# Performance work log

Hardware: AMD Instinct MI355X
Metric: run time of the kernel (lower is better)

## Reference

```python
import jax, jax.numpy as jnp
import numpy as np

HIDDEN = 2048
INTER = 4096
HEADS = 32
HEAD_DIM = INTER // HEADS  # 128
STATE = 128
GROUPS = 1
CONV_K = 4
CHUNK = 256
EPS = 1e-5
CONV_DIM = INTER + 2 * GROUPS * STATE  # 4352
DT_MIN, DT_MAX = 0.0, 100.0
BATCH, SEQ = 2, 4096


def _segment_sum(x):
    """Stable segment sum: returns (..., T, T) with entry [i,j] = sum_{k=j+1..i} x[k] (-inf above diag)."""
    T = x.shape[-1]
    xx = jnp.broadcast_to(x[..., None], x.shape + (T,))
    mask_lower = jnp.tril(jnp.ones((T, T), bool), -1)
    xx = jnp.where(mask_lower, xx, 0.0)
    seg = jnp.cumsum(xx, axis=-2)
    mask_incl = jnp.tril(jnp.ones((T, T), bool), 0)
    return jnp.where(mask_incl, seg, -jnp.inf)


def setup_inputs() -> dict:
    key = jax.random.key(0)
    ks = jax.random.split(key, 8)
    std = 0.02
    return {
        "hidden_states": jax.random.normal(ks[0], (BATCH, SEQ, HIDDEN), jnp.float32),
        "in_proj_w": jax.random.normal(ks[1], (INTER + CONV_DIM + HEADS, HIDDEN), jnp.float32) * std,
        "conv_w": jax.random.normal(ks[2], (CONV_DIM, 1, CONV_K), jnp.float32) * std,
        "conv_b": jnp.zeros((CONV_DIM,), jnp.float32),
        "A_log": jnp.log(jax.random.uniform(ks[3], (HEADS,), jnp.float32, 1.0, 16.0)),
        "dt_bias": jax.random.normal(ks[4], (HEADS,), jnp.float32) * 0.1,
        "D": jnp.ones((HEADS,), jnp.float32),
        "norm_w": jnp.ones((INTER,), jnp.float32),
        "out_proj_w": jax.random.normal(ks[5], (HIDDEN, INTER), jnp.float32) * (std / np.sqrt(48.0)),
    }


def reference(hidden_states, in_proj_w, conv_w, conv_b, A_log, dt_bias, D, norm_w, out_proj_w):
    b, s, _ = hidden_states.shape
    # in_proj and split into gate / conv-input / dt
    proj = hidden_states @ in_proj_w.T
    gate, hBC, dt = jnp.split(proj, [INTER, INTER + CONV_DIM], axis=-1)

    # causal depthwise conv1d (padding k-1 left, truncate to seq_len) + SiLU
    x = jnp.transpose(hBC, (0, 2, 1))  # (b, conv_dim, s)
    x = jax.lax.conv_general_dilated(
        x, conv_w, window_strides=(1,), padding=[(CONV_K - 1, 0)],
        dimension_numbers=("NCH", "OIH", "NCH"), feature_group_count=CONV_DIM)
    x = x + conv_b[None, :, None]
    hBC = jax.nn.silu(jnp.transpose(x, (0, 2, 1)))  # (b, s, conv_dim)

    xs, B, C = jnp.split(hBC, [INTER, INTER + GROUPS * STATE], axis=-1)

    A = -jnp.exp(A_log)  # (h,)
    dt = jnp.clip(jax.nn.softplus(dt + dt_bias), DT_MIN, DT_MAX)  # (b, s, h)

    xs = xs.reshape(b, s, HEADS, HEAD_DIM)
    rep = HEADS // GROUPS
    Bm = jnp.repeat(B.reshape(b, s, GROUPS, STATE), rep, axis=2)  # (b,s,h,n)
    Cm = jnp.repeat(C.reshape(b, s, GROUPS, STATE), rep, axis=2)

    pad = (-s) % CHUNK

    def padseq(t):
        return jnp.pad(t, ((0, 0), (0, pad)) + ((0, 0),) * (t.ndim - 2))

    D_res = D[None, None, :, None] * padseq(xs)  # (b, S, h, p)
    xdt = padseq(xs * dt[..., None])
    Ad = padseq(A[None, None, :] * dt)  # (b, S, h)
    Bm, Cm = padseq(Bm), padseq(Cm)

    nc = (s + pad) // CHUNK
    xdt = xdt.reshape(b, nc, CHUNK, HEADS, HEAD_DIM)
    Ad = jnp.transpose(Ad.reshape(b, nc, CHUNK, HEADS), (0, 3, 1, 2))  # (b,h,c,l)
    Bm = Bm.reshape(b, nc, CHUNK, HEADS, STATE)
    Cm = Cm.reshape(b, nc, CHUNK, HEADS, STATE)

    A_cum = jnp.cumsum(Ad, axis=-1)  # (b,h,c,l)

    # 1) intra-chunk (diagonal block) output
    L = jnp.exp(_segment_sum(Ad))  # (b,h,c,l,l)
    G = jnp.einsum("bclhn,bcshn->bclsh", Cm, Bm)
    M = G * jnp.transpose(L, (0, 2, 3, 4, 1))
    Y_diag = jnp.einsum("bclsh,bcshp->bclhp", M, xdt)

    # 2) per-chunk final states
    decay_states = jnp.exp(A_cum[:, :, :, -1:] - A_cum)  # (b,h,c,l)
    B_decay = Bm * jnp.transpose(decay_states, (0, 2, 3, 1))[..., None]
    states = jnp.einsum("bclhn,bclhp->bchpn", B_decay, xdt)  # (b,c,h,p,n)

    # 3) inter-chunk recurrence
    states = jnp.concatenate([jnp.zeros_like(states[:, :1]), states], axis=1)  # (b,c+1,h,p,n)
    chunk_sums = jnp.pad(A_cum[:, :, :, -1], ((0, 0), (0, 0), (1, 0)))  # (b,h,c+1)
    decay_chunk = jnp.exp(_segment_sum(chunk_sums))  # (b,h,c+1,c+1)
    decay_chunk = jnp.transpose(decay_chunk, (0, 2, 3, 1))  # (b,c,z,h)
    new_states = jnp.einsum("bczh,bchpn->bzhpn", decay_chunk, states)
    states = new_states[:, :-1]  # (b,c,h,p,n) state entering each chunk

    # 4) state -> output contribution
    state_decay = jnp.exp(A_cum)  # (b,h,c,l)
    Y_off = jnp.einsum("bclhn,bchpn->bclhp", Cm, states) * jnp.transpose(state_decay, (0, 2, 3, 1))[..., None]

    y = (Y_diag + Y_off).reshape(b, nc * CHUNK, HEADS, HEAD_DIM) + D_res
    y = y[:, :s].reshape(b, s, INTER)

    # gated RMSNorm
    y = y * jax.nn.silu(gate)
    var = jnp.mean(y * y, axis=-1, keepdims=True)
    y = y * jax.lax.rsqrt(var + EPS) * norm_w

    return y @ out_proj_w.T
```

## Files before the change

kernel.cpp:

```cpp
#include <hip/hip_runtime.h>

#define SEQ     4096
#define BATCH   2
#define NROWS   8192
#define HID     2048
#define INTER_  4096
#define NHEADS  32
#define HDIM    128
#define NSTATE  128
#define CDIM    4352
#define NPROJ_  8480
#define NPAD    8704
#define NCH     16
#define CHUNK_  256

typedef __attribute__((ext_vector_type(8))) short bf16x8;
typedef __attribute__((ext_vector_type(4))) short short4v;
typedef __attribute__((ext_vector_type(4))) float f32x4;

#define AS1 __attribute__((address_space(1)))
#define AS3 __attribute__((address_space(3)))

__device__ __forceinline__ float bf2f(short s) {
  union { unsigned u; float f; } x;
  x.u = ((unsigned)(unsigned short)s) << 16;
  return x.f;
}
__device__ __forceinline__ short f2bf(float f) {
  union { float f; unsigned u; } x; x.f = f;
  unsigned r = x.u + 0x7FFFu + ((x.u >> 16) & 1u);
  return (short)(r >> 16);
}

__global__ void cvt_bf16(const float* __restrict__ in, short* __restrict__ out,
                         int n4, int nsrc4) {
  int i = blockIdx.x * 256 + threadIdx.x;
  if (i >= n4) return;
  short4v o = {0, 0, 0, 0};
  if (i < nsrc4) {
    f32x4 v = *(const f32x4*)(in + (size_t)i * 4);
    o = (short4v){ f2bf(v.x), f2bf(v.y), f2bf(v.z), f2bf(v.w) };
  }
  *(short4v*)(out + (size_t)i * 4) = o;
}

template<int MODE>
__global__ __launch_bounds__(512, 4)
void gemm256(const short* __restrict__ A, const short* __restrict__ Bw,
             int M, int N, int K, int nM,
             float* __restrict__ outF, short* __restrict__ gate,
             short* __restrict__ hbc, float* __restrict__ dtraw)
{
  __shared__ __align__(16) short ldsA[3][256 * 32];
  __shared__ __align__(16) short ldsB[3][128 * 32];
  const int tid = threadIdx.x;
  const int lane = tid & 63, wave = tid >> 6;
  const int l16 = lane & 15, lhi = lane >> 4;
  const int wm = wave >> 1, wn = wave & 1;

  const int bm = blockIdx.x % nM, bn = blockIdx.x / nM;
  const size_t row0 = (size_t)bm * 256;
  const int    col0 = bn * 128;

  const short* Ab  = A + row0 * K;
  const short* Bbp = Bw + (size_t)col0 * K;

  f32x4 acc[4][4];
  #pragma unroll
  for (int m = 0; m < 4; ++m)
    #pragma unroll
    for (int n = 0; n < 4; ++n) acc[m][n] = (f32x4){0.f, 0.f, 0.f, 0.f};

  auto stage = [&](int s) {
    int sl = s % 3;
    short* sa = &ldsA[sl][0];
    short* sb = &ldsB[sl][0];
    int ko = s * 32;
    #pragma unroll
    for (int j = 0; j < 2; ++j) {
      int u = j * 512 + tid;
      int r = u >> 2;
      int q = (u & 3) ^ ((r >> 1) & 3);
      __builtin_amdgcn_global_load_lds(
          (const AS1 unsigned*)(Ab + (size_t)r * K + ko + q * 8),
          (AS3 unsigned*)(sa + (j * 512 + wave * 64) * 8), 16, 0, 0);
    }
    {
      int r = tid >> 2;
      int q = (tid & 3) ^ ((r >> 1) & 3);
      __builtin_amdgcn_global_load_lds(
          (const AS1 unsigned*)(Bbp + (size_t)r * K + ko + q * 8),
          (AS3 unsigned*)(sb + wave * 64 * 8), 16, 0, 0);
    }
  };

  auto compute = [&](int s) {
    int sl = s % 3;
    const short* sa = &ldsA[sl][0];
    const short* sb = &ldsB[sl][0];
    bf16x8 a[4], b[4];
    #pragma unroll
    for (int mf = 0; mf < 4; ++mf) {
      int rr = wm * 64 + mf * 16 + l16;
      int q = lhi ^ ((rr >> 1) & 3);
      a[mf] = *(const bf16x8*)(sa + rr * 32 + q * 8);
    }
    #pragma unroll
    for (int nf = 0; nf < 4; ++nf) {
      int rr = wn * 64 + nf * 16 + l16;
      int q = lhi ^ ((rr >> 1) & 3);
      b[nf] = *(const bf16x8*)(sb + rr * 32 + q * 8);
    }
    __builtin_amdgcn_s_setprio(1);
    #pragma unroll
    for (int mf = 0; mf < 4; ++mf)
      #pragma unroll
      for (int nf = 0; nf < 4; ++nf)
        acc[mf][nf] = __builtin_amdgcn_mfma_f32_16x16x32_bf16(a[mf], b[nf], acc[mf][nf], 0, 0, 0);
    __builtin_amdgcn_s_setprio(0);
  };

  const int ns = K / 32;
  stage(0); stage(1);
  asm volatile("s_waitcnt vmcnt(3)" ::: "memory");
  __builtin_amdgcn_s_barrier();

  for (int s = 0; s < ns; ++s) {
    if (s + 2 < ns) stage(s + 2);
    compute(s);
    if (s + 1 < ns) {
      if (s + 2 < ns) asm volatile("s_waitcnt vmcnt(3)" ::: "memory");
      else            asm volatile("s_waitcnt vmcnt(0)" ::: "memory");
      __builtin_amdgcn_s_barrier();
    }
  }

  #pragma unroll
  for (int mf = 0; mf < 4; ++mf) {
    #pragma unroll
    for (int nf = 0; nf < 4; ++nf) {
      #pragma unroll
      for (int j = 0; j < 4; ++j) {
        int gr = (int)row0 + wm * 64 + mf * 16 + lhi * 4 + j;
        int gc = col0 + wn * 64 + nf * 16 + l16;
        float v = acc[mf][nf][j];
        if (MODE == 0) {
          outF[(size_t)gr * N + gc] = v;
        } else {
          if (gc < INTER_)             gate[(size_t)gr * INTER_ + gc] = f2bf(v);
          else if (gc < INTER_ + CDIM) hbc[(size_t)gr * CDIM + (gc - INTER_)] = f2bf(v);
          else if (gc < NPROJ_)        dtraw[(size_t)gr * NHEADS + (gc - INTER_ - CDIM)] = v;
        }
      }
    }
  }
}

__global__ __launch_bounds__(256)
void conv_t(const short* __restrict__ hbc, const float* __restrict__ cw,
            const float* __restrict__ cb, short* __restrict__ xsT,
            short* __restrict__ Bb, short* __restrict__ Cb, short* __restrict__ BbT)
{
  __shared__ short sOut[64][130];
  int ct = blockIdx.y;
  int cl = threadIdx.x & 127;
  int rh = threadIdx.x >> 7;
  int c = ct * 128 + cl;
  int row0 = blockIdx.x * 64;
  int s0 = row0 & (SEQ - 1);
  float w0 = cw[c * 4 + 0], w1 = cw[c * 4 + 1], w2 = cw[c * 4 + 2], w3 = cw[c * 4 + 3];
  float bias = cb[c];
  int r0 = rh * 32;
  float h0, h1, h2;
  h0 = (s0 + r0 - 3 >= 0) ? bf2f(hbc[(size_t)(row0 + r0 - 3) * CDIM + c]) : 0.f;
  h1 = (s0 + r0 - 2 >= 0) ? bf2f(hbc[(size_t)(row0 + r0 - 2) * CDIM + c]) : 0.f;
  h2 = (s0 + r0 - 1 >= 0) ? bf2f(hbc[(size_t)(row0 + r0 - 1) * CDIM + c]) : 0.f;

  for (int r = r0; r < r0 + 32; ++r) {
    float xin = bf2f(hbc[(size_t)(row0 + r) * CDIM + c]);
    float a = bias + w0 * h0 + w1 * h1 + w2 * h2 + w3 * xin;
    h0 = h1; h1 = h2; h2 = xin;
    float v = a / (1.f + expf(-a));
    short bv = f2bf(v);
    if (ct < 33) sOut[r][cl] = bv;
    if (ct == 32)      Bb[(size_t)(row0 + r) * NSTATE + cl] = bv;
    else if (ct == 33) Cb[(size_t)(row0 + r) * NSTATE + cl] = bv;
  }
  if (ct >= 33) return;
  __syncthreads();
  int p = threadIdx.x >> 1, sh = (threadIdx.x & 1) * 32;
  int b = row0 >> 12;
  size_t dst;
  short* outp;
  if (ct < 32) { outp = xsT; dst = ((size_t)(b * 32 + ct) * 128 + p) * SEQ + s0 + sh; }
  else         { outp = BbT; dst = ((size_t)b * 128 + p) * SEQ + s0 + sh; }
  #pragma unroll
  for (int g = 0; g < 8; ++g) {
    short4v o;
    o[0] = sOut[sh + g * 4 + 0][p];
    o[1] = sOut[sh + g * 4 + 1][p];
    o[2] = sOut[sh + g * 4 + 2][p];
    o[3] = sOut[sh + g * 4 + 3][p];
    *(short4v*)(outp + dst + g * 4) = o;
  }
}

__global__ void dt_proc(const float* __restrict__ dtraw, const float* __restrict__ dtb,
                        float* __restrict__ dtT, int n) {
  int i = blockIdx.x * 256 + threadIdx.x;
  if (i >= n) return;
  float x = dtraw[i] + dtb[i & (NHEADS - 1)];
  float sp = (x > 20.f) ? x : log1pf(expf(x));
  float d = fminf(fmaxf(sp, 0.f), 100.f);
  int row = i >> 5, h = i & 31;
  dtT[(size_t)h * NROWS + row] = d;
}

__global__ __launch_bounds__(256)
void ssm_state(const short* __restrict__ xsT, const short* __restrict__ BbT,
               const float* __restrict__ dtT, const float* __restrict__ Alog,
               float* __restrict__ cs, float* __restrict__ dAsum)
{
  int blk = blockIdx.x;
  int h = blk & 31, cc = (blk >> 5) & 15, b = blk >> 9;
  int tid = threadIdx.x, lane = tid & 63, wave = tid >> 6;
  int l16 = lane & 15, lhi = lane >> 4;
  int s0 = cc * CHUNK_;

  __shared__ float acum[256];
  __shared__ float sdt[256];
  { float Ah = -expf(Alog[h]);
    float d = dtT[(size_t)h * NROWS + (size_t)b * SEQ + s0 + tid];
    sdt[tid] = d; acum[tid] = Ah * d; }
  for (int off = 1; off < 256; off <<= 1) {
    __syncthreads();
    float v = (tid >= off) ? acum[tid - off] : 0.f;
    __syncthreads();
    acum[tid] += v;
  }
  __syncthreads();
  float alast = acum[255];

  const short* xbase = xsT + ((size_t)(b * 32 + h) * 128) * SEQ + s0;
  const short* bbase = BbT + ((size_t)b * 128) * SEQ + s0;

  f32x4 acc[2][8];
  #pragma unroll
  for (int m = 0; m < 2; ++m)
    #pragma unroll
    for (int n = 0; n < 8; ++n) acc[m][n] = (f32x4){0.f, 0.f, 0.f, 0.f};

  for (int lt0 = 0; lt0 < 256; lt0 += 32) {
    float fe[8];
    #pragma unroll
    for (int e = 0; e < 8; ++e) {
      int kl = lt0 + lhi * 8 + e;
      fe[e] = sdt[kl] * __expf(alast - acum[kl]);
    }
    bf16x8 af[2];
    #pragma unroll
    for (int m = 0; m < 2; ++m) {
      bf16x8 raw = *(const bf16x8*)(xbase + (size_t)(wave * 32 + m * 16 + l16) * SEQ + lt0 + lhi * 8);
      bf16x8 sc;
      #pragma unroll
      for (int e = 0; e < 8; ++e) sc[e] = f2bf(bf2f(raw[e]) * fe[e]);
      af[m] = sc;
    }
    #pragma unroll
    for (int n = 0; n < 8; ++n) {
      bf16x8 bfv = *(const bf16x8*)(bbase + (size_t)(n * 16 + l16) * SEQ + lt0 + lhi * 8);
      acc[0][n] = __builtin_amdgcn_mfma_f32_16x16x32_bf16(af[0], bfv, acc[0][n], 0, 0, 0);
      acc[1][n] = __builtin_amdgcn_mfma_f32_16x16x32_bf16(af[1], bfv, acc[1][n], 0, 0, 0);
    }
  }
  size_t base = (size_t)blk * 16384;
  #pragma unroll
  for (int m = 0; m < 2; ++m)
    #pragma unroll
    for (int n = 0; n < 8; ++n)
      #pragma unroll
      for (int j = 0; j < 4; ++j) {
        int p = wave * 32 + m * 16 + lhi * 4 + j;
        int ng = n * 16 + l16;
        cs[base + (size_t)p * NSTATE + ng] = acc[m][n][j];
      }
  if (tid == 0) dAsum[blk] = alast;
}

__global__ void ssm_scan(float* __restrict__ cs, const float* __restrict__ dAsum) {
  int idx = blockIdx.x * 256 + threadIdx.x;
  int np = idx & 16383;
  int bh = idx >> 14;
  int h = bh & 31, b = bh >> 5;
  float run = 0.f;
  #pragma unroll
  for (int c = 0; c < NCH; ++c) {
    size_t base = ((size_t)((b * NCH + c) * NHEADS + h)) * 16384 + np;
    float v = cs[base];
    cs[base] = run;
    run = run * __expf(dAsum[(b * NCH + c) * NHEADS + h]) + v;
  }
}

__global__ __launch_bounds__(256)
void ssm_y(const short* __restrict__ xsT, const short* __restrict__ Bb,
           const short* __restrict__ Cb, const float* __restrict__ dtT,
           const float* __restrict__ Alog, const float* __restrict__ Dv,
           const float* __restrict__ cs, short* __restrict__ gateY)
{
  int blk = blockIdx.y, lt = blockIdx.x;
  int h = blk & 31, cc = (blk >> 5) & 15, b = blk >> 9;
  int tid = threadIdx.x, lane = tid & 63, wave = tid >> 6;
  int l16 = lane & 15, lhi = lane >> 4;
  int s0 = cc * CHUNK_;
  size_t row0 = (size_t)b * SEQ + s0;

  __shared__ float acum[256];
  __shared__ float sdt[256];
  __shared__ __align__(16) short M_lds[64 * 264];

  { float Ah = -expf(Alog[h]);
    float d = dtT[(size_t)h * NROWS + row0 + tid];
    sdt[tid] = d; acum[tid] = Ah * d; }
  for (int off = 1; off < 256; off <<= 1) {
    __syncthreads();
    float v = (tid >= off) ? acum[tid - off] : 0.f;
    __syncthreads();
    acum[tid] += v;
  }
  __syncthreads();

  float Dh = Dv[h];

  {
    f32x4 acc1[4][4];
    #pragma unroll
    for (int m = 0; m < 4; ++m)
      #pragma unroll
      for (int n = 0; n < 4; ++n) acc1[m][n] = (f32x4){0.f, 0.f, 0.f, 0.f};
    for (int kk = 0; kk < NSTATE; kk += 32) {
      bf16x8 af[4], bv[4];
      #pragma unroll
      for (int m = 0; m < 4; ++m)
        af[m] = *(const bf16x8*)(Cb + (row0 + lt * 64 + m * 16 + l16) * NSTATE + kk + lhi * 8);
      #pragma unroll
      for (int n = 0; n < 4; ++n)
        bv[n] = *(const bf16x8*)(Bb + (row0 + wave * 64 + n * 16 + l16) * NSTATE + kk + lhi * 8);
      #pragma unroll
      for (int m = 0; m < 4; ++m)
        #pragma unroll
        for (int n = 0; n < 4; ++n)
          acc1[m][n] = __builtin_amdgcn_mfma_f32_16x16x32_bf16(af[m], bv[n], acc1[m][n], 0, 0, 0);
    }
    float as_[4]; int sg_[4];
    #pragma unroll
    for (int n = 0; n < 4; ++n) { sg_[n] = wave * 64 + n * 16 + l16; as_[n] = acum[sg_[n]]; }
    #pragma unroll
    for (int m = 0; m < 4; ++m) {
      #pragma unroll
      for (int j = 0; j < 4; ++j) {
        int ll = m * 16 + lhi * 4 + j;
        int lg = lt * 64 + ll;
        float al = acum[lg];
        float dinv = Dh / fmaxf(sdt[lg], 1e-20f);
        #pragma unroll
        for (int n = 0; n < 4; ++n) {
          float v = 0.f;
          if (sg_[n] <= lg) {
            v = acc1[m][n][j] * __expf(al - as_[n]);
            if (sg_[n] == lg) v += dinv;
          }
          M_lds[ll * 264 + wave * 64 + n * 16 + l16] = f2bf(v);
        }
      }
    }
  }
  __syncthreads();

  const short* xbase = xsT + ((size_t)(b * 32 + h) * 128) * SEQ + s0;

  f32x4 accY[4][2];
  #pragma unroll
  for (int m = 0; m < 4; ++m) { accY[m][0] = (f32x4){0,0,0,0}; accY[m][1] = (f32x4){0,0,0,0}; }
  int smax = (lt + 1) * 64;
  for (int st = 0; st < smax; st += 32) {
    float fe[8];
    #pragma unroll
    for (int e = 0; e < 8; ++e) fe[e] = sdt[st + lhi * 8 + e];
    bf16x8 bv2[2];
    #pragma unroll
    for (int n = 0; n < 2; ++n) {
      bf16x8 raw = *(const bf16x8*)(xbase + (size_t)(wave * 32 + n * 16 + l16) * SEQ + st + lhi * 8);
      bf16x8 sc;
      #pragma unroll
      for (int e = 0; e < 8; ++e) sc[e] = f2bf(bf2f(raw[e]) * fe[e]);
      bv2[n] = sc;
    }
    #pragma unroll
    for (int m = 0; m < 4; ++m) {
      bf16x8 a = *(const bf16x8*)(M_lds + (m * 16 + l16) * 264 + st + lhi * 8);
      accY[m][0] = __builtin_amdgcn_mfma_f32_16x16x32_bf16(a, bv2[0], accY[m][0], 0, 0, 0);
      accY[m][1] = __builtin_amdgcn_mfma_f32_16x16x32_bf16(a, bv2[1], accY[m][1], 0, 0, 0);
    }
  }

  f32x4 accO[4][2];
  #pragma unroll
  for (int m = 0; m < 4; ++m) { accO[m][0] = (f32x4){0,0,0,0}; accO[m][1] = (f32x4){0,0,0,0}; }
  size_t pbase = (size_t)blk * 16384;
  for (int nt = 0; nt < NSTATE; nt += 32) {
    bf16x8 bv2[2];
    #pragma unroll
    for (int n = 0; n < 2; ++n) {
      int p = wave * 32 + n * 16 + l16;
      const float* src = cs + pbase + (size_t)p * NSTATE + nt + lhi * 8;
      f32x4 v0 = *(const f32x4*)src;
      f32x4 v1 = *(const f32x4*)(src + 4);
      bf16x8 sc;
      sc[0] = f2bf(v0.x); sc[1] = f2bf(v0.y); sc[2] = f2bf(v0.z); sc[3] = f2bf(v0.w);
      sc[4] = f2bf(v1.x); sc[5] = f2bf(v1.y); sc[6] = f2bf(v1.z); sc[7] = f2bf(v1.w);
      bv2[n] = sc;
    }
    #pragma unroll
    for (int m = 0; m < 4; ++m) {
      bf16x8 a = *(const bf16x8*)(Cb + (row0 + lt * 64 + m * 16 + l16) * NSTATE + nt + lhi * 8);
      accO[m][0] = __builtin_amdgcn_mfma_f32_16x16x32_bf16(a, bv2[0], accO[m][0], 0, 0, 0);
      accO[m][1] = __builtin_amdgcn_mfma_f32_16x16x32_bf16(a, bv2[1], accO[m][1], 0, 0, 0);
    }
  }

  #pragma unroll
  for (int m = 0; m < 4; ++m) {
    #pragma unroll
    for (int j = 0; j < 4; ++j) {
      int ll = m * 16 + lhi * 4 + j;
      float e = __expf(acum[lt * 64 + ll]);
      size_t row = row0 + lt * 64 + ll;
      #pragma unroll
      for (int n = 0; n < 2; ++n) {
        int p = wave * 32 + n * 16 + l16;
        size_t adr = row * INTER_ + h * HDIM + p;
        float yv = accY[m][n][j] + e * accO[m][n][j];
        float g = bf2f(gateY[adr]);
        gateY[adr] = f2bf(yv * g / (1.f + expf(-g)));
      }
    }
  }
}

__global__ __launch_bounds__(256)
void gate_norm(short* __restrict__ ybf, const float* __restrict__ nw)
{
  int row = blockIdx.x;
  int tid = threadIdx.x;
  size_t base = (size_t)row * INTER_;
  float vals[16];
  float ss = 0.f;
  #pragma unroll
  for (int i = 0; i < 16; ++i) {
    int idx = tid + i * 256;
    float v = bf2f(ybf[base + idx]);
    vals[i] = v;
    ss += v * v;
  }
  #pragma unroll
  for (int off = 32; off > 0; off >>= 1) ss += __shfl_down(ss, off);
  __shared__ float ws4[4];
  if ((tid & 63) == 0) ws4[tid >> 6] = ss;
  __syncthreads();
  float tot = ws4[0] + ws4[1] + ws4[2] + ws4[3];
  float scale = rsqrtf(tot * (1.f / 4096.f) + 1e-5f);
  #pragma unroll
  for (int i = 0; i < 16; ++i) {
    int idx = tid + i * 256;
    ybf[base + idx] = f2bf(vals[i] * scale * nw[idx]);
  }
}

extern "C" void kernel_launch(void* const* d_in, const int* in_sizes, int n_in,
                              void* d_out, int out_size, void* d_ws, size_t ws_size,
                              hipStream_t stream)
{
  const float* Xf   = (const float*)d_in[0];
  const float* W1f  = (const float*)d_in[1];
  const float* cw   = (const float*)d_in[2];
  const float* cb   = (const float*)d_in[3];
  const float* Alog = (const float*)d_in[4];
  const float* dtb  = (const float*)d_in[5];
  const float* Dv   = (const float*)d_in[6];
  const float* nw   = (const float*)d_in[7];
  const float* W2f  = (const float*)d_in[8];
  float* outp = (float*)d_out;
  char* ws = (char*)d_ws;

  size_t off = 0;
  short* Xb  = (short*)(ws + off); off += (size_t)NROWS * HID * 2;
  short* W1b = (short*)(ws + off); off += (size_t)NPAD * HID * 2;
  short* xsT = (short*)ws;
  short* W2b = (short*)(ws + off); off += (size_t)HID * INTER_ * 2;
  short* gateY = (short*)(ws + off); off += (size_t)NROWS * INTER_ * 2;
  short* hbc  = (short*)(ws + off); off += (size_t)NROWS * CDIM * 2;
  float* dtv  = (float*)(ws + off); off += (size_t)NROWS * NHEADS * 4;
  float* dtT  = (float*)(ws + off); off += (size_t)NROWS * NHEADS * 4;
  short* Bb   = (short*)(ws + off); off += (size_t)NROWS * NSTATE * 2;
  short* Cb   = (short*)(ws + off); off += (size_t)NROWS * NSTATE * 2;
  short* BbT  = (short*)(ws + off); off += (size_t)NROWS * NSTATE * 2;
  float* dAs  = (float*)(ws + off); off += 4096;
  float* cs   = (float*)hbc;

  cvt_bf16<<<(NROWS * HID / 4 + 255) / 256, 256, 0, stream>>>(
      Xf, Xb, NROWS * HID / 4, NROWS * HID / 4);
  cvt_bf16<<<(NPAD * HID / 4 + 255) / 256, 256, 0, stream>>>(
      W1f, W1b, NPAD * HID / 4, NPROJ_ * HID / 4);
  cvt_bf16<<<(HID * INTER_ / 4 + 255) / 256, 256, 0, stream>>>(
      W2f, W2b, HID * INTER_ / 4, HID * INTER_ / 4);

  gemm256<1><<<(NROWS / 256) * (NPAD / 128), 512, 0, stream>>>(
      Xb, W1b, NROWS, NPROJ_, HID, NROWS / 256, nullptr, gateY, hbc, dtv);

  dt_proc<<<(NROWS * NHEADS) / 256, 256, 0, stream>>>(dtv, dtb, dtT, NROWS * NHEADS);
  conv_t<<<dim3(NROWS / 64, 34), 256, 0, stream>>>(hbc, cw, cb, xsT, Bb, Cb, BbT);

  ssm_state<<<BATCH * NCH * NHEADS, 256, 0, stream>>>(xsT, BbT, dtT, Alog, cs, dAs);
  ssm_scan<<<(BATCH * NHEADS * 16384) / 256, 256, 0, stream>>>(cs, dAs);
  ssm_y<<<dim3(4, BATCH * NCH * NHEADS), 256, 0, stream>>>(xsT, Bb, Cb, dtT, Alog, Dv, cs, gateY);

  gate_norm<<<NROWS, 256, 0, stream>>>(gateY, nw);

  gemm256<0><<<(NROWS / 256) * (HID / 128), 512, 0, stream>>>(
      gateY, W2b, NROWS, HID, INTER_, NROWS / 256, outp, nullptr, nullptr, nullptr);
}
```

Before: 906.2 us.

## Enlarge GEMM tile to 256x256 with K=64 double-buffered interleaved pipeline

Both projection GEMMs now use 256x256 output tiles, with each of 8 waves computing 128x64 instead of 64x64. Each k-step covers 64, held as two 32-wide halves for A and B, and the kernel double-buffers whole k-steps. Global-to-LDS prefetch of the next tile is split across sub-phases so it overlaps the MFMA work. The larger tile raises arithmetic intensity and cuts global traffic per FLOP. In exchange it uses more registers and 128KB of LDS, so only one block fits per CU, launch bounds drop to 1, and the grid becomes smaller with more barriers per step.

```diff
diff --git a/kernel.cpp b/kernel.cpp
--- a/kernel.cpp
+++ b/kernel.cpp
@@ -45,111 +45,120 @@
 }
 
 template<int MODE>
-__global__ __launch_bounds__(512, 4)
+__global__ __launch_bounds__(512, 1)
 void gemm256(const short* __restrict__ A, const short* __restrict__ Bw,
              int M, int N, int K, int nM,
              float* __restrict__ outF, short* __restrict__ gate,
              short* __restrict__ hbc, float* __restrict__ dtraw)
 {
-  __shared__ __align__(16) short ldsA[3][256 * 32];
-  __shared__ __align__(16) short ldsB[3][128 * 32];
+  __shared__ __align__(16) short lds[2][2][2][256 * 32];
   const int tid = threadIdx.x;
   const int lane = tid & 63, wave = tid >> 6;
   const int l16 = lane & 15, lhi = lane >> 4;
-  const int wm = wave >> 1, wn = wave & 1;
+  const int wm = wave >> 2, wn = wave & 3;
 
   const int bm = blockIdx.x % nM, bn = blockIdx.x / nM;
   const size_t row0 = (size_t)bm * 256;
-  const int    col0 = bn * 128;
+  const int    col0 = bn * 256;
 
   const short* Ab  = A + row0 * K;
   const short* Bbp = Bw + (size_t)col0 * K;
 
-  f32x4 acc[4][4];
-  #pragma unroll
-  for (int m = 0; m < 4; ++m)
+  f32x4 acc[8][4];
+  #pragma unroll
+  for (int m = 0; m < 8; ++m)
     #pragma unroll
     for (int n = 0; n < 4; ++n) acc[m][n] = (f32x4){0.f, 0.f, 0.f, 0.f};
 
-  auto stage = [&](int s) {
-    int sl = s % 3;
-    short* sa = &ldsA[sl][0];
-    short* sb = &ldsB[sl][0];
-    int ko = s * 32;
+  auto stage = [&](int bufq, int mat, int kh, int ko) {
+    const short* gsrc = mat ? Bbp : Ab;
+    short* base = &lds[bufq][mat][kh][0];
     #pragma unroll
     for (int j = 0; j < 2; ++j) {
       int u = j * 512 + tid;
       int r = u >> 2;
-      int q = (u & 3) ^ ((r >> 1) & 3);
+      int g = (u & 3) ^ ((r >> 1) & 3);
       __builtin_amdgcn_global_load_lds(
-          (const AS1 unsigned*)(Ab + (size_t)r * K + ko + q * 8),
-          (AS3 unsigned*)(sa + (j * 512 + wave * 64) * 8), 16, 0, 0);
-    }
-    {
-      int r = tid >> 2;
-      int q = (tid & 3) ^ ((r >> 1) & 3);
-      __builtin_amdgcn_global_load_lds(
-          (const AS1 unsigned*)(Bbp + (size_t)r * K + ko + q * 8),
-          (AS3 unsigned*)(sb + wave * 64 * 8), 16, 0, 0);
+          (const AS1 unsigned*)(gsrc + (size_t)r * K + ko + kh * 32 + g * 8),
+          (AS3 unsigned*)(base + (j * 512 + wave * 64) * 8), 16, 0, 0);
     }
   };
-
-  auto compute = [&](int s) {
-    int sl = s % 3;
-    const short* sa = &ldsA[sl][0];
-    const short* sb = &ldsB[sl][0];
-    bf16x8 a[4], b[4];
-    #pragma unroll
-    for (int mf = 0; mf < 4; ++mf) {
-      int rr = wm * 64 + mf * 16 + l16;
-      int q = lhi ^ ((rr >> 1) & 3);
-      a[mf] = *(const bf16x8*)(sa + rr * 32 + q * 8);
-    }
-    #pragma unroll
-    for (int nf = 0; nf < 4; ++nf) {
-      int rr = wn * 64 + nf * 16 + l16;
-      int q = lhi ^ ((rr >> 1) & 3);
-      b[nf] = *(const bf16x8*)(sb + rr * 32 + q * 8);
-    }
-    __builtin_amdgcn_s_setprio(1);
-    #pragma unroll
-    for (int mf = 0; mf < 4; ++mf)
-      #pragma unroll
-      for (int nf = 0; nf < 4; ++nf)
-        acc[mf][nf] = __builtin_amdgcn_mfma_f32_16x16x32_bf16(a[mf], b[nf], acc[mf][nf], 0, 0, 0);
-    __builtin_amdgcn_s_setprio(0);
+  auto readA = [&](int bufq, int kh, int mh, bf16x8* a) {
+    const short* base = &lds[bufq][0][kh][0];
+    #pragma unroll
+    for (int f = 0; f < 4; ++f) {
+      int rr = wm * 128 + mh * 64 + f * 16 + l16;
+      int g = lhi ^ ((rr >> 1) & 3);
+      a[f] = *(const bf16x8*)(base + rr * 32 + g * 8);
+    }
   };
-
-  const int ns = K / 32;
-  stage(0); stage(1);
-  asm volatile("s_waitcnt vmcnt(3)" ::: "memory");
+  auto readB = [&](int bufq, int kh, bf16x8* b) {
+    const short* base = &lds[bufq][1][kh][0];
+    #pragma unroll
+    for (int f = 0; f < 4; ++f) {
+      int rr = wn * 64 + f * 16 + l16;
+      int g = lhi ^ ((rr >> 1) & 3);
+      b[f] = *(const bf16x8*)(base + rr * 32 + g * 8);
+    }
+  };
+
+  const int nt = K / 64;
+  stage(0, 0, 0, 0); stage(0, 1, 0, 0); stage(0, 0, 1, 0); stage(0, 1, 1, 0);
+  asm volatile("s_waitcnt vmcnt(4)" ::: "memory");
   __builtin_amdgcn_s_barrier();
 
-  for (int s = 0; s < ns; ++s) {
-    if (s + 2 < ns) stage(s + 2);
-    compute(s);
-    if (s + 1 < ns) {
-      if (s + 2 < ns) asm volatile("s_waitcnt vmcnt(3)" ::: "memory");
-      else            asm volatile("s_waitcnt vmcnt(0)" ::: "memory");
-      __builtin_amdgcn_s_barrier();
-    }
-  }
-
-  #pragma unroll
-  for (int mf = 0; mf < 4; ++mf) {
-    #pragma unroll
-    for (int nf = 0; nf < 4; ++nf) {
-      #pragma unroll
-      for (int j = 0; j < 4; ++j) {
-        int gr = (int)row0 + wm * 64 + mf * 16 + lhi * 4 + j;
-        int gc = col0 + wn * 64 + nf * 16 + l16;
-        float v = acc[mf][nf][j];
-        if (MODE == 0) {
-          outF[(size_t)gr * N + gc] = v;
-        } else {
-          if (gc < INTER_)             gate[(size_t)gr * INTER_ + gc] = f2bf(v);
-          else if (gc < INTER_ + CDIM) hbc[(size_t)gr * CDIM + (gc - INTER_)] = f2bf(v);
-          else if (gc < NPROJ_)        dtraw[(size_t)gr * NHEADS + (gc - INTER_ - CDIM)] = v;
+  for (int t = 0; t < nt; ++t) {
+    const int buf = t & 1, nb = buf ^ 1;
+    const int kon = (t + 1) * 64;
+    const bool pf = (t + 1 < nt);
+    bf16x8 bfr[4];
+
+    #pragma unroll
+    for (int kh = 0; kh < 2; ++kh) {
+      #pragma unroll
+      for (int mh = 0; mh < 2; ++mh) {
+        bf16x8 a[4];
+        if (mh == 0) readB(buf, kh, bfr);
+        readA(buf, kh, mh, a);
+        if (pf) stage(nb, mh, kh, kon);
+        __builtin_amdgcn_s_barrier();
+        asm volatile("s_waitcnt lgkmcnt(0)" ::: "memory");
+        __builtin_amdgcn_sched_barrier(0);
+        __builtin_amdgcn_s_setprio(1);
+        #pragma unroll
+        for (int f = 0; f < 4; ++f)
+          #pragma unroll
+          for (int nf = 0; nf < 4; ++nf)
+            acc[mh * 4 + f][nf] =
+                __builtin_amdgcn_mfma_f32_16x16x32_bf16(a[f], bfr[nf], acc[mh * 4 + f][nf], 0, 0, 0);
+        __builtin_amdgcn_s_setprio(0);
+        if (mh == 1) {
+          if (pf) asm volatile("s_waitcnt vmcnt(4)" ::: "memory");
+          else    asm volatile("s_waitcnt vmcnt(0)" ::: "memory");
+        }
+        __builtin_amdgcn_s_barrier();
+      }
+    }
+  }
+
+  #pragma unroll
+  for (int mh = 0; mh < 2; ++mh) {
+    #pragma unroll
+    for (int f = 0; f < 4; ++f) {
+      #pragma unroll
+      for (int nf = 0; nf < 4; ++nf) {
+        #pragma unroll
+        for (int j = 0; j < 4; ++j) {
+          int gr = (int)row0 + wm * 128 + mh * 64 + f * 16 + lhi * 4 + j;
+          int gc = col0 + wn * 64 + nf * 16 + l16;
+          float v = acc[mh * 4 + f][nf][j];
+          if (MODE == 0) {
+            outF[(size_t)gr * N + gc] = v;
+          } else {
+            if (gc < INTER_)             gate[(size_t)gr * INTER_ + gc] = f2bf(v);
+            else if (gc < INTER_ + CDIM) hbc[(size_t)gr * CDIM + (gc - INTER_)] = f2bf(v);
+            else if (gc < NPROJ_)        dtraw[(size_t)gr * NHEADS + (gc - INTER_ - CDIM)] = v;
+          }
         }
       }
     }
@@ -515,7 +524,7 @@
   cvt_bf16<<<(HID * INTER_ / 4 + 255) / 256, 256, 0, stream>>>(
       W2f, W2b, HID * INTER_ / 4, HID * INTER_ / 4);
 
-  gemm256<1><<<(NROWS / 256) * (NPAD / 128), 512, 0, stream>>>(
+  gemm256<1><<<(NROWS / 256) * (NPAD / 256), 512, 0, stream>>>(
       Xb, W1b, NROWS, NPROJ_, HID, NROWS / 256, nullptr, gateY, hbc, dtv);
 
   dt_proc<<<(NROWS * NHEADS) / 256, 256, 0, stream>>>(dtv, dtb, dtT, NROWS * NHEADS);
@@ -527,6 +536,6 @@
 
   gate_norm<<<NROWS, 256, 0, stream>>>(gateY, nw);
 
-  gemm256<0><<<(NROWS / 256) * (HID / 128), 512, 0, stream>>>(
+  gemm256<0><<<(NROWS / 256) * (HID / 256), 512, 0, stream>>>(
       gateY, W2b, NROWS, HID, INTER_, NROWS / 256, outp, nullptr, nullptr, nullptr);
 }
```

Result: no change. 900.7 us (-0.6%).
